# Performance work log

Hardware: AMD Instinct MI355X
Metric: run time of the kernel (lower is better)

The kernel has to match this reference:

```python
import jax, jax.numpy as jnp
import numpy as np

B = 4096          # players (batch)
DEG = 64          # asteroids per player
A = B * DEG       # total asteroids
E = A             # one edge per asteroid (asteroid -> its player)
PD, AD, ED = 5, 3, 7
HID = 64
HEADS = 4
OUT = HID         # GATv2Conv out_channels (concat=False -> mean over heads)
L = 2             # num_layers
NEG_SLOPE = 0.2
LN_EPS = 1e-5


def setup_inputs() -> dict:
    key = jax.random.key(0)
    ks = jax.random.split(key, 20)
    f = jnp.float32
    inp = {}
    inp["player_feat"] = jax.random.normal(ks[0], (B, PD), f)
    inp["asteroid_feat"] = jax.random.normal(ks[1], (A, AD), f)
    src = jnp.arange(E, dtype=jnp.int32)
    dst = src // DEG                      # player batch index per edge
    inp["edge_index"] = jnp.stack([src, dst])  # [2, E] int32
    inp["edge_attr"] = jax.random.normal(ks[2], (E, ED), f)
    sc = 0.1
    # input projections
    inp["Wp"] = jax.random.normal(ks[3], (PD, HID), f) * sc
    inp["bp"] = jnp.zeros((HID,), f)
    inp["Wa"] = jax.random.normal(ks[4], (AD, HID), f) * sc
    inp["ba"] = jnp.zeros((HID,), f)
    # per-layer GATv2 params (stacked over L)
    inp["Wl"] = jax.random.normal(ks[5], (L, HID, HEADS * OUT), f) * sc
    inp["bl"] = jnp.zeros((L, HEADS * OUT), f)
    inp["Wr"] = jax.random.normal(ks[6], (L, HID, HEADS * OUT), f) * sc
    inp["br"] = jnp.zeros((L, HEADS * OUT), f)
    inp["We"] = jax.random.normal(ks[7], (L, ED, HEADS * OUT), f) * sc
    inp["att"] = jax.random.normal(ks[8], (L, HEADS, OUT), f) * sc
    inp["bias"] = jnp.zeros((L, OUT), f)
    inp["ln_g"] = jnp.ones((L, HID), f)
    inp["ln_b"] = jnp.zeros((L, HID), f)
    return inp


def _layer_norm(x, g, b):
    mu = jnp.mean(x, axis=-1, keepdims=True)
    var = jnp.mean(jnp.square(x - mu), axis=-1, keepdims=True)
    return (x - mu) * jax.lax.rsqrt(var + LN_EPS) * g + b


def _gatv2(x, src, dst, edge_attr, Wl, bl, Wr, br, We, att, bias, n_nodes):
    # x: [N, HID]; src/dst: [E]; PyG GATv2Conv, add_self_loops=False, concat=False
    xl = (x @ Wl + bl).reshape(-1, HEADS, OUT)   # source transform
    xr = (x @ Wr + br).reshape(-1, HEADS, OUT)   # target transform
    ea = (edge_attr @ We).reshape(-1, HEADS, OUT)
    e = xl[src] + xr[dst] + ea                   # [E, H, O]
    e = jnp.where(e >= 0, e, NEG_SLOPE * e)      # LeakyReLU(0.2)
    logits = jnp.einsum('eho,ho->eh', e, att)    # [E, H]
    # segment softmax over incoming edges of each target node
    m = jax.ops.segment_max(logits, dst, num_segments=n_nodes)
    al = jnp.exp(logits - m[dst])
    den = jax.ops.segment_sum(al, dst, num_segments=n_nodes)
    alpha = al / den[dst]                        # [E, H]
    msg = alpha[:, :, None] * xl[src]            # [E, H, O]
    out = jax.ops.segment_sum(msg, dst, num_segments=n_nodes)  # [N, H, O]
    return jnp.mean(out, axis=1) + bias          # concat=False -> head mean


def reference(player_feat, asteroid_feat, edge_index, edge_attr,
              Wp, bp, Wa, ba, Wl, bl, Wr, br, We, att, bias, ln_g, ln_b):
    batch = player_feat.shape[0]
    h_p = jax.nn.relu(player_feat @ Wp + bp)
    h_a = jax.nn.relu(asteroid_feat @ Wa + ba)
    x = jnp.concatenate([h_p, h_a], axis=0)      # [N, HID]
    n_nodes = x.shape[0]
    src = edge_index[0] + batch                  # asteroid local -> global idx
    dst = edge_index[1]
    for i in range(L):
        x_new = _gatv2(x, src, dst, edge_attr, Wl[i], bl[i], Wr[i], br[i],
                       We[i], att[i], bias[i], n_nodes)
        x = _layer_norm(x + jax.nn.relu(x_new), ln_g[i], ln_b[i])
    return x[:batch]
```

## Files before the change

kernel.cpp:

```cpp
#include <hip/hip_runtime.h>


typedef __bf16 bf16x8 __attribute__((ext_vector_type(8)));
typedef float  f32x4  __attribute__((ext_vector_type(4)));

union FragU { unsigned short u[8]; bf16x8 v; };

__device__ __forceinline__ float bf2f(unsigned short u) {
    union { unsigned int i; float f; } v; v.i = ((unsigned int)u) << 16; return v.f;
}
__device__ __forceinline__ unsigned short f2bf(float f) {
    union { __bf16 b; unsigned short u; } x; x.b = (__bf16)f; return x.u;
}

#define NEG_SLOPE 0.2f
#define LN_EPS 1e-5f
#define XS 72

struct Smem {
    __align__(16) unsigned short xa[4][64 * XS];
    __align__(16) unsigned short xpb[4][64];
    __align__(16) float alf[4][256];
    float outp[4][256];
    float xp[4][64];
    float afs[4][192];
    float rbs[64], gs[64], bs[64];
};

#define WS_NEED (163840 + 3 * 8192)

__global__ __launch_bounds__(256) void prep_weights(
    const float* __restrict__ Wl, const float* __restrict__ Wr,
    const float* __restrict__ We, const float* __restrict__ bl,
    const float* __restrict__ att, const float* __restrict__ br,
    unsigned short* __restrict__ wlf, unsigned short* __restrict__ wrf,
    unsigned short* __restrict__ wef, f32x4* __restrict__ blq,
    f32x4* __restrict__ attq, f32x4* __restrict__ brq)
{
    int g = blockIdx.x * 256 + threadIdx.x;
    {
        int layer = (g >> 11) & 1, frag = (g >> 8) & 7, t = g & 255;
        int nt = frag >> 1, ko = frag & 1;
        int c = (t >> 6) * 64 + nt * 16 + (t & 15);
        int kb = ko * 32 + ((t >> 4) & 3) * 8;
        const float* srcL = Wl + layer * 16384 + kb * 256 + c;
        const float* srcR = Wr + layer * 16384 + kb * 256 + c;
        FragU fl, fr;
        #pragma unroll
        for (int jj = 0; jj < 8; ++jj) {
            fl.u[jj] = f2bf(srcL[jj * 256]);
            fr.u[jj] = f2bf(srcR[jj * 256]);
        }
        *reinterpret_cast<bf16x8*>(&wlf[g * 8]) = fl.v;
        *reinterpret_cast<bf16x8*>(&wrf[g * 8]) = fr.v;
    }
    if (g < 2048) {
        int l2 = (g >> 10) & 1, n2 = (g >> 8) & 3, t2 = g & 255;
        int q2 = (t2 >> 4) & 3;
        int c2 = (t2 >> 6) * 64 + n2 * 16 + (t2 & 15);
        FragU fe;
        #pragma unroll
        for (int j2 = 0; j2 < 8; ++j2)
            fe.u[j2] = (q2 == 0 && j2 < 7) ? f2bf(We[l2 * 1792 + j2 * 256 + c2])
                                           : (unsigned short)0;
        *reinterpret_cast<bf16x8*>(&wef[g * 8]) = fe.v;
    }
    if (g < 512) {
        int lyr = g >> 8, tt = g & 255;
        int hb = (tt >> 6) * 64, mm = tt & 15;
        f32x4 b, a, r;
        #pragma unroll
        for (int n = 0; n < 4; ++n) {
            int cc = hb + n * 16 + mm;
            b[n] = bl[lyr * 256 + cc];
            a[n] = att[lyr * 256 + cc];
            r[n] = br[lyr * 256 + cc];
        }
        blq[g] = b; attq[g] = a; brq[g] = r;
    }
}

template <bool WS>
__global__ __launch_bounds__(256) void gnn_main(
    const float* __restrict__ pf, const float* __restrict__ af,
    const float* __restrict__ eat, const float* __restrict__ Wp,
    const float* __restrict__ bp, const float* __restrict__ Wa,
    const float* __restrict__ ba, const float* __restrict__ Wl,
    const float* __restrict__ bl, const float* __restrict__ Wr,
    const float* __restrict__ br, const float* __restrict__ We,
    const float* __restrict__ att, const float* __restrict__ bias,
    const float* __restrict__ lng, const float* __restrict__ lnb,
    const unsigned short* __restrict__ wlf, const unsigned short* __restrict__ wrf,
    const unsigned short* __restrict__ wef, const f32x4* __restrict__ blq,
    const f32x4* __restrict__ attq, const f32x4* __restrict__ brq,
    float* __restrict__ out)
{
    __shared__ Smem sm;
    const int p0 = blockIdx.x * 4, t = threadIdx.x;
    const int w = t >> 6, l = t & 63, q = l >> 4, m = l & 15;
    const int cbase = w * 64;

    #pragma unroll
    for (int it = 0; it < 3; ++it) {
        int idx = it * 256 + t;
        int pl = idx / 192, o = idx - pl * 192;
        sm.afs[pl][o] = af[(p0 + pl) * 192 + o];
    }
    if (t < 64) {
        sm.rbs[t] = fmaxf(bias[t], 0.f);
        sm.gs[t] = lng[t];
        sm.bs[t] = lnb[t];
    }
    {
        int pl = w, tt = l;
        float acc = bp[tt];
        #pragma unroll
        for (int d = 0; d < 5; ++d) acc += pf[(p0 + pl) * 5 + d] * Wp[d * 64 + tt];
        float xp0 = fmaxf(acc, 0.f);
        sm.xp[pl][tt] = xp0;
        sm.xpb[pl][tt] = f2bf(xp0);
    }
    __syncthreads();
    {
        const int pl = w, k = l;
        float wa0 = Wa[k], wa1 = Wa[64 + k], wa2 = Wa[128 + k], bak = ba[k];
        #pragma unroll
        for (int j = 0; j < 64; ++j) {
            float acc = bak + sm.afs[pl][j * 3] * wa0 + sm.afs[pl][j * 3 + 1] * wa1
                      + sm.afs[pl][j * 3 + 2] * wa2;
            sm.xa[pl][j * XS + k] = f2bf(fmaxf(acc, 0.f));
        }
    }
    #pragma unroll
    for (int it = 0; it < 8; ++it) {
        int idx = it * 256 + t;
        int pl = idx >> 9, jd = idx & 511, j = jd >> 3, d = jd & 7;
        sm.xa[pl][j * XS + 64 + d] = (d < 7) ? f2bf(eat[((p0 + pl) * 64 + j) * 7 + d])
                                             : (unsigned short)0;
    }
    __syncthreads();

    for (int layer = 0; layer < 2; ++layer) {
        f32x4 blv, atv, brv;
        if constexpr (WS) {
            blv = blq[layer * 256 + t];
            atv = attq[layer * 256 + t];
            brv = brq[layer * 256 + t];
        } else {
            #pragma unroll
            for (int nt = 0; nt < 4; ++nt) {
                int c = cbase + nt * 16 + m;
                blv[nt] = bl[layer * 256 + c];
                atv[nt] = att[layer * 256 + c];
                brv[nt] = br[layer * 256 + c];
            }
        }

        float bx[4][4];
        {
            FragU xf0[4], xf1[4];
            #pragma unroll
            for (int pl = 0; pl < 4; ++pl) {
                xf0[pl].v = *reinterpret_cast<const bf16x8*>(&sm.xpb[pl][q * 8]);
                xf1[pl].v = *reinterpret_cast<const bf16x8*>(&sm.xpb[pl][32 + q * 8]);
            }
            #pragma unroll
            for (int nt = 0; nt < 4; ++nt) {
                FragU r0, r1;
                if constexpr (WS) {
                    r0.v = *reinterpret_cast<const bf16x8*>(&wrf[((layer * 8 + nt * 2 + 0) * 256 + t) * 8]);
                    r1.v = *reinterpret_cast<const bf16x8*>(&wrf[((layer * 8 + nt * 2 + 1) * 256 + t) * 8]);
                } else {
                    int c = cbase + nt * 16 + m;
                    #pragma unroll
                    for (int jj = 0; jj < 8; ++jj) {
                        r0.u[jj] = f2bf(Wr[layer * 16384 + (q * 8 + jj) * 256 + c]);
                        r1.u[jj] = f2bf(Wr[layer * 16384 + (32 + q * 8 + jj) * 256 + c]);
                    }
                }
                #pragma unroll
                for (int pl = 0; pl < 4; ++pl) {
                    f32x4 cx = { brv[nt], brv[nt], brv[nt], brv[nt] };
                    cx = __builtin_amdgcn_mfma_f32_16x16x32_bf16(xf0[pl].v, r0.v, cx, 0, 0, 0);
                    cx = __builtin_amdgcn_mfma_f32_16x16x32_bf16(xf1[pl].v, r1.v, cx, 0, 0, 0);
                    bx[pl][nt] = blv[nt] + cx[0];
                }
            }
        }

        FragU bfr[8];
        bf16x8 ebf[4];
        if constexpr (WS) {
            #pragma unroll
            for (int f = 0; f < 8; ++f)
                bfr[f].v = *reinterpret_cast<const bf16x8*>(&wlf[((layer * 8 + f) * 256 + t) * 8]);
            #pragma unroll
            for (int nt = 0; nt < 4; ++nt)
                ebf[nt] = *reinterpret_cast<const bf16x8*>(&wef[((layer * 4 + nt) * 256 + t) * 8]);
        } else {
            const float* Wli = Wl + layer * 16384;
            #pragma unroll
            for (int nt = 0; nt < 4; ++nt) {
                int c = cbase + nt * 16 + m;
                #pragma unroll
                for (int ko = 0; ko < 2; ++ko) {
                    int kb = ko * 32 + q * 8;
                    #pragma unroll
                    for (int jj = 0; jj < 8; ++jj)
                        bfr[nt * 2 + ko].u[jj] = f2bf(Wli[(kb + jj) * 256 + c]);
                }
                FragU e;
                #pragma unroll
                for (int jj = 0; jj < 8; ++jj)
                    e.u[jj] = (q == 0 && jj < 7) ? f2bf(We[layer * 1792 + jj * 256 + c])
                                                 : (unsigned short)0;
                ebf[nt] = e.v;
            }
        }

        const bool b0 = (m & 1) != 0, b1 = (m & 2) != 0;
        const bool b2 = (m & 4) != 0, b3 = (m & 8) != 0;
        float P[4][4];
        #pragma unroll
        for (int mt = 0; mt < 4; ++mt) {
            const int row = mt * 16 + m;
            #pragma unroll
            for (int pl = 0; pl < 4; ++pl) {
                bf16x8 a0 = *reinterpret_cast<const bf16x8*>(&sm.xa[pl][row * XS + q * 8]);
                bf16x8 a1 = *reinterpret_cast<const bf16x8*>(&sm.xa[pl][row * XS + 32 + q * 8]);
                bf16x8 a2 = *reinterpret_cast<const bf16x8*>(&sm.xa[pl][row * XS + 64]);
                float lp4[4] = { 0.f, 0.f, 0.f, 0.f };
                #pragma unroll
                for (int nt = 0; nt < 4; ++nt) {
                    f32x4 acc = { bx[pl][nt], bx[pl][nt], bx[pl][nt], bx[pl][nt] };
                    acc = __builtin_amdgcn_mfma_f32_16x16x32_bf16(a0, bfr[nt * 2 + 0].v, acc, 0, 0, 0);
                    acc = __builtin_amdgcn_mfma_f32_16x16x32_bf16(a1, bfr[nt * 2 + 1].v, acc, 0, 0, 0);
                    f32x4 ef = __builtin_amdgcn_mfma_f32_16x16x32_bf16(a2, ebf[nt], acc, 0, 0, 0);
                    #pragma unroll
                    for (int r = 0; r < 4; ++r) {
                        float ev = ef[r];
                        ev = fmaxf(ev, NEG_SLOPE * ev);
                        lp4[r] += ev * atv[nt];
                    }
                }
                float e0k = b0 ? lp4[1] : lp4[0], e0s = b0 ? lp4[0] : lp4[1];
                float ea = e0k + __shfl_xor(e0s, 1, 64);
                float e1k = b0 ? lp4[3] : lp4[2], e1s = b0 ? lp4[2] : lp4[3];
                float eb = e1k + __shfl_xor(e1s, 1, 64);
                float fk = b1 ? eb : ea, fs = b1 ? ea : eb;
                P[pl][mt] = fk + __shfl_xor(fs, 2, 64);
            }
        }

        float rden[4];
        #pragma unroll
        for (int pl = 0; pl < 4; ++pl) {
            float g0k = b2 ? P[pl][1] : P[pl][0], g0s = b2 ? P[pl][0] : P[pl][1];
            float ga = g0k + __shfl_xor(g0s, 4, 64);
            float g1k = b2 ? P[pl][3] : P[pl][2], g1s = b2 ? P[pl][2] : P[pl][3];
            float gb = g1k + __shfl_xor(g1s, 4, 64);
            float hk = b3 ? gb : ga, hs = b3 ? ga : gb;
            float lg = hk + __shfl_xor(hs, 8, 64);
            float al = __expf(lg);
            float den = al;
            #pragma unroll
            for (int msk = 1; msk <= 32; msk <<= 1) den += __shfl_xor(den, msk, 64);
            rden[pl] = 1.f / den;
            const int rj = ((m >> 2) * 16) + (q * 4) + (m & 3);
            sm.alf[pl][w * 64 + rj] = al;
        }
        __builtin_amdgcn_wave_barrier();

        #pragma unroll
        for (int pl = 0; pl < 4; ++pl) {
            const f32x4* alv = reinterpret_cast<const f32x4*>(&sm.alf[pl][cbase]);
            f32x4 al4[4];
            #pragma unroll
            for (int mt = 0; mt < 4; ++mt) al4[mt] = alv[mt * 4 + q];
            float s[4] = { 0.f, 0.f, 0.f, 0.f };
            #pragma unroll
            for (int mt = 0; mt < 4; ++mt) {
                const int row = mt * 16 + m;
                bf16x8 a0 = *reinterpret_cast<const bf16x8*>(&sm.xa[pl][row * XS + q * 8]);
                bf16x8 a1 = *reinterpret_cast<const bf16x8*>(&sm.xa[pl][row * XS + 32 + q * 8]);
                #pragma unroll
                for (int nt = 0; nt < 4; ++nt) {
                    f32x4 c1 = { bx[pl][nt], bx[pl][nt], bx[pl][nt], bx[pl][nt] };
                    c1 = __builtin_amdgcn_mfma_f32_16x16x32_bf16(a0, bfr[nt * 2 + 0].v, c1, 0, 0, 0);
                    c1 = __builtin_amdgcn_mfma_f32_16x16x32_bf16(a1, bfr[nt * 2 + 1].v, c1, 0, 0, 0);
                    s[nt] += al4[mt][0] * c1[0] + al4[mt][1] * c1[1]
                           + al4[mt][2] * c1[2] + al4[mt][3] * c1[3];
                }
            }
            #pragma unroll
            for (int nt = 0; nt < 4; ++nt) {
                float sv = s[nt];
                sv += __shfl_xor(sv, 16, 64);
                sv += __shfl_xor(sv, 32, 64);
                if (q == 0)
                    sm.outp[pl][cbase + nt * 16 + m] = sv * rden[pl] - (bx[pl][nt] - blv[nt]);
            }
        }
        __syncthreads();

        if (layer == 0) {
            #pragma unroll
            for (int half = 0; half < 2; ++half) {
                const int g = t >> 1, pl = half * 2 + (g >> 6), j = g & 63, part = t & 1;
                unsigned short* rowp = &sm.xa[pl][j * XS + part * 32];
                FragU A0, A1, A2, A3;
                A0.v = *reinterpret_cast<const bf16x8*>(rowp);
                A1.v = *reinterpret_cast<const bf16x8*>(rowp + 8);
                A2.v = *reinterpret_cast<const bf16x8*>(rowp + 16);
                A3.v = *reinterpret_cast<const bf16x8*>(rowp + 24);
                float v[32], sum = 0.f, sq = 0.f;
                #pragma unroll
                for (int i = 0; i < 32; ++i) {
                    unsigned short us = (i < 8) ? A0.u[i] : (i < 16) ? A1.u[i - 8]
                                      : (i < 24) ? A2.u[i - 16] : A3.u[i - 24];
                    float x = bf2f(us) + sm.rbs[part * 32 + i];
                    v[i] = x; sum += x; sq += x * x;
                }
                sum += __shfl_xor(sum, 1, 64); sq += __shfl_xor(sq, 1, 64);
                float mu = sum * (1.f / 64.f);
                float var = sq * (1.f / 64.f) - mu * mu;
                float rs = rsqrtf(var + LN_EPS);
                FragU O0, O1, O2, O3;
                #pragma unroll
                for (int i = 0; i < 32; ++i) {
                    int col = part * 32 + i;
                    unsigned short ub = f2bf((v[i] - mu) * rs * sm.gs[col] + sm.bs[col]);
                    if (i < 8) O0.u[i] = ub;
                    else if (i < 16) O1.u[i - 8] = ub;
                    else if (i < 24) O2.u[i - 16] = ub;
                    else O3.u[i - 24] = ub;
                }
                *reinterpret_cast<bf16x8*>(rowp) = O0.v;
                *reinterpret_cast<bf16x8*>(rowp + 8) = O1.v;
                *reinterpret_cast<bf16x8*>(rowp + 16) = O2.v;
                *reinterpret_cast<bf16x8*>(rowp + 24) = O3.v;
            }
            {
                const int pl = w, tt = l;
                float xnew = 0.25f * (sm.outp[pl][tt] + sm.outp[pl][64 + tt]
                                    + sm.outp[pl][128 + tt] + sm.outp[pl][192 + tt])
                           + bias[tt];
                float v = sm.xp[pl][tt] + fmaxf(xnew, 0.f);
                float sum = v, sq = v * v;
                #pragma unroll
                for (int msk = 1; msk <= 32; msk <<= 1) {
                    sum += __shfl_xor(sum, msk, 64);
                    sq  += __shfl_xor(sq,  msk, 64);
                }
                float mu = sum * (1.f / 64.f);
                float var = sq * (1.f / 64.f) - mu * mu;
                float y = (v - mu) * rsqrtf(var + LN_EPS) * lng[tt] + lnb[tt];
                sm.xp[pl][tt] = y;
                sm.xpb[pl][tt] = f2bf(y);
            }
            __syncthreads();
        } else {
            {
                const int pl = w, tt = l;
                float xnew = 0.25f * (sm.outp[pl][tt] + sm.outp[pl][64 + tt]
                                    + sm.outp[pl][128 + tt] + sm.outp[pl][192 + tt])
                           + bias[64 + tt];
                float v = sm.xp[pl][tt] + fmaxf(xnew, 0.f);
                float sum = v, sq = v * v;
                #pragma unroll
                for (int msk = 1; msk <= 32; msk <<= 1) {
                    sum += __shfl_xor(sum, msk, 64);
                    sq  += __shfl_xor(sq,  msk, 64);
                }
                float mu = sum * (1.f / 64.f);
                float var = sq * (1.f / 64.f) - mu * mu;
                float y = (v - mu) * rsqrtf(var + LN_EPS) * lng[64 + tt] + lnb[64 + tt];
                out[(p0 + pl) * 64 + tt] = y;
            }
        }
    }
}

extern "C" void kernel_launch(void* const* d_in, const int* in_sizes, int n_in,
                              void* d_out, int out_size, void* d_ws, size_t ws_size,
                              hipStream_t stream) {
    const float* pf   = (const float*)d_in[0];
    const float* af   = (const float*)d_in[1];
    const float* eat  = (const float*)d_in[3];
    const float* Wp   = (const float*)d_in[4];
    const float* bp   = (const float*)d_in[5];
    const float* Wa   = (const float*)d_in[6];
    const float* ba   = (const float*)d_in[7];
    const float* Wl   = (const float*)d_in[8];
    const float* bl   = (const float*)d_in[9];
    const float* Wr   = (const float*)d_in[10];
    const float* br   = (const float*)d_in[11];
    const float* We   = (const float*)d_in[12];
    const float* att  = (const float*)d_in[13];
    const float* bias = (const float*)d_in[14];
    const float* lng  = (const float*)d_in[15];
    const float* lnb  = (const float*)d_in[16];
    float* out = (float*)d_out;

    const int B = in_sizes[0] / 5;
    unsigned short* wlf = (unsigned short*)d_ws;
    unsigned short* wrf = wlf + 32768;
    unsigned short* wef = wrf + 32768;
    f32x4* blq  = (f32x4*)((char*)d_ws + 163840);
    f32x4* attq = blq + 512;
    f32x4* brq  = attq + 512;

    if (ws_size >= WS_NEED) {
        prep_weights<<<dim3(16), dim3(256), 0, stream>>>(
            Wl, Wr, We, bl, att, br, wlf, wrf, wef, blq, attq, brq);
        gnn_main<true><<<dim3(B / 4), dim3(256), 0, stream>>>(
            pf, af, eat, Wp, bp, Wa, ba, Wl, bl, Wr, br, We, att, bias, lng, lnb,
            wlf, wrf, wef, blq, attq, brq, out);
    } else {
        gnn_main<false><<<dim3(B / 4), dim3(256), 0, stream>>>(
            pf, af, eat, Wp, bp, Wa, ba, Wl, bl, Wr, br, We, att, bias, lng, lnb,
            wlf, wrf, wef, blq, attq, brq, out);
    }
}
```

Before: 164.6 us.

## Assign one player per wave, looping over heads to drop block-level syncs

Result: slower. 179.1 us (+8.8%).

```diff
diff --git a/kernel.cpp b/kernel.cpp
--- a/kernel.cpp
+++ b/kernel.cpp
@@ -20,8 +20,7 @@
 struct Smem {
     __align__(16) unsigned short xa[4][64 * XS];
     __align__(16) unsigned short xpb[4][64];
-    __align__(16) float alf[4][256];
-    float outp[4][256];
+    __align__(16) float alf[4][64];
     float xp[4][64];
     float afs[4][192];
     float rbs[64], gs[64], bs[64];
@@ -98,141 +97,134 @@
     __shared__ Smem sm;
     const int p0 = blockIdx.x * 4, t = threadIdx.x;
     const int w = t >> 6, l = t & 63, q = l >> 4, m = l & 15;
-    const int cbase = w * 64;
-
-    #pragma unroll
-    for (int it = 0; it < 3; ++it) {
-        int idx = it * 256 + t;
-        int pl = idx / 192, o = idx - pl * 192;
-        sm.afs[pl][o] = af[(p0 + pl) * 192 + o];
-    }
+    const int p = p0 + w;
+
     if (t < 64) {
         sm.rbs[t] = fmaxf(bias[t], 0.f);
         sm.gs[t] = lng[t];
         sm.bs[t] = lnb[t];
     }
+    #pragma unroll
+    for (int it = 0; it < 3; ++it)
+        sm.afs[w][it * 64 + l] = af[p * 192 + it * 64 + l];
     {
-        int pl = w, tt = l;
-        float acc = bp[tt];
+        float acc = bp[l];
         #pragma unroll
-        for (int d = 0; d < 5; ++d) acc += pf[(p0 + pl) * 5 + d] * Wp[d * 64 + tt];
+        for (int d = 0; d < 5; ++d) acc += pf[p * 5 + d] * Wp[d * 64 + l];
         float xp0 = fmaxf(acc, 0.f);
-        sm.xp[pl][tt] = xp0;
-        sm.xpb[pl][tt] = f2bf(xp0);
-    }
-    __syncthreads();
+        sm.xp[w][l] = xp0;
+        sm.xpb[w][l] = f2bf(xp0);
+    }
+    __builtin_amdgcn_wave_barrier();
     {
-        const int pl = w, k = l;
+        const int k = l;
         float wa0 = Wa[k], wa1 = Wa[64 + k], wa2 = Wa[128 + k], bak = ba[k];
         #pragma unroll
         for (int j = 0; j < 64; ++j) {
-            float acc = bak + sm.afs[pl][j * 3] * wa0 + sm.afs[pl][j * 3 + 1] * wa1
-                      + sm.afs[pl][j * 3 + 2] * wa2;
-            sm.xa[pl][j * XS + k] = f2bf(fmaxf(acc, 0.f));
+            float acc = bak + sm.afs[w][j * 3] * wa0 + sm.afs[w][j * 3 + 1] * wa1
+                      + sm.afs[w][j * 3 + 2] * wa2;
+            sm.xa[w][j * XS + k] = f2bf(fmaxf(acc, 0.f));
         }
     }
     #pragma unroll
     for (int it = 0; it < 8; ++it) {
-        int idx = it * 256 + t;
-        int pl = idx >> 9, jd = idx & 511, j = jd >> 3, d = jd & 7;
-        sm.xa[pl][j * XS + 64 + d] = (d < 7) ? f2bf(eat[((p0 + pl) * 64 + j) * 7 + d])
-                                             : (unsigned short)0;
+        int idx = it * 64 + l, j = idx >> 3, d = idx & 7;
+        sm.xa[w][j * XS + 64 + d] = (d < 7) ? f2bf(eat[(p * 64 + j) * 7 + d])
+                                            : (unsigned short)0;
     }
     __syncthreads();
 
+    const bool b0 = (m & 1) != 0, b1 = (m & 2) != 0;
+    const bool b2 = (m & 4) != 0, b3 = (m & 8) != 0;
+
     for (int layer = 0; layer < 2; ++layer) {
-        f32x4 blv, atv, brv;
-        if constexpr (WS) {
-            blv = blq[layer * 256 + t];
-            atv = attq[layer * 256 + t];
-            brv = brq[layer * 256 + t];
-        } else {
-            #pragma unroll
-            for (int nt = 0; nt < 4; ++nt) {
-                int c = cbase + nt * 16 + m;
-                blv[nt] = bl[layer * 256 + c];
-                atv[nt] = att[layer * 256 + c];
-                brv[nt] = br[layer * 256 + c];
-            }
-        }
-
-        float bx[4][4];
-        {
-            FragU xf0[4], xf1[4];
-            #pragma unroll
-            for (int pl = 0; pl < 4; ++pl) {
-                xf0[pl].v = *reinterpret_cast<const bf16x8*>(&sm.xpb[pl][q * 8]);
-                xf1[pl].v = *reinterpret_cast<const bf16x8*>(&sm.xpb[pl][32 + q * 8]);
-            }
-            #pragma unroll
-            for (int nt = 0; nt < 4; ++nt) {
-                FragU r0, r1;
-                if constexpr (WS) {
-                    r0.v = *reinterpret_cast<const bf16x8*>(&wrf[((layer * 8 + nt * 2 + 0) * 256 + t) * 8]);
-                    r1.v = *reinterpret_cast<const bf16x8*>(&wrf[((layer * 8 + nt * 2 + 1) * 256 + t) * 8]);
-                } else {
-                    int c = cbase + nt * 16 + m;
+        float macc[4] = { 0.f, 0.f, 0.f, 0.f };
+
+        for (int h = 0; h < 4; ++h) {
+            const int ti = h * 64 + l;
+
+            f32x4 blv, atv, brv;
+            if constexpr (WS) {
+                blv = blq[layer * 256 + ti];
+                atv = attq[layer * 256 + ti];
+                brv = brq[layer * 256 + ti];
+            } else {
+                #pragma unroll
+                for (int nt = 0; nt < 4; ++nt) {
+                    int c = h * 64 + nt * 16 + m;
+                    blv[nt] = bl[layer * 256 + c];
+                    atv[nt] = att[layer * 256 + c];
+                    brv[nt] = br[layer * 256 + c];
+                }
+            }
+
+            float bxv[4];
+            {
+                FragU xf0, xf1;
+                xf0.v = *reinterpret_cast<const bf16x8*>(&sm.xpb[w][q * 8]);
+                xf1.v = *reinterpret_cast<const bf16x8*>(&sm.xpb[w][32 + q * 8]);
+                #pragma unroll
+                for (int nt = 0; nt < 4; ++nt) {
+                    FragU r0, r1;
+                    if constexpr (WS) {
+                        r0.v = *reinterpret_cast<const bf16x8*>(&wrf[((layer * 8 + nt * 2 + 0) * 256 + ti) * 8]);
+                        r1.v = *reinterpret_cast<const bf16x8*>(&wrf[((layer * 8 + nt * 2 + 1) * 256 + ti) * 8]);
+                    } else {
+                        int c = h * 64 + nt * 16 + m;
+                        #pragma unroll
+                        for (int jj = 0; jj < 8; ++jj) {
+                            r0.u[jj] = f2bf(Wr[layer * 16384 + (q * 8 + jj) * 256 + c]);
+                            r1.u[jj] = f2bf(Wr[layer * 16384 + (32 + q * 8 + jj) * 256 + c]);
+                        }
+                    }
+                    f32x4 cx = { brv[nt], brv[nt], brv[nt], brv[nt] };
+                    cx = __builtin_amdgcn_mfma_f32_16x16x32_bf16(xf0.v, r0.v, cx, 0, 0, 0);
+                    cx = __builtin_amdgcn_mfma_f32_16x16x32_bf16(xf1.v, r1.v, cx, 0, 0, 0);
+                    bxv[nt] = blv[nt] + cx[0];
+                }
+            }
+
+            FragU bfr[8];
+            bf16x8 ebf[4];
+            if constexpr (WS) {
+                #pragma unroll
+                for (int f = 0; f < 8; ++f)
+                    bfr[f].v = *reinterpret_cast<const bf16x8*>(&wlf[((layer * 8 + f) * 256 + ti) * 8]);
+                #pragma unroll
+                for (int nt = 0; nt < 4; ++nt)
+                    ebf[nt] = *reinterpret_cast<const bf16x8*>(&wef[((layer * 4 + nt) * 256 + ti) * 8]);
+            } else {
+                const float* Wli = Wl + layer * 16384;
+                #pragma unroll
+                for (int nt = 0; nt < 4; ++nt) {
+                    int c = h * 64 + nt * 16 + m;
                     #pragma unroll
-                    for (int jj = 0; jj < 8; ++jj) {
-                        r0.u[jj] = f2bf(Wr[layer * 16384 + (q * 8 + jj) * 256 + c]);
-                        r1.u[jj] = f2bf(Wr[layer * 16384 + (32 + q * 8 + jj) * 256 + c]);
+                    for (int ko = 0; ko < 2; ++ko) {
+                        int kb = ko * 32 + q * 8;
+                        #pragma unroll
+                        for (int jj = 0; jj < 8; ++jj)
+                            bfr[nt * 2 + ko].u[jj] = f2bf(Wli[(kb + jj) * 256 + c]);
                     }
-                }
-                #pragma unroll
-                for (int pl = 0; pl < 4; ++pl) {
-                    f32x4 cx = { brv[nt], brv[nt], brv[nt], brv[nt] };
-                    cx = __builtin_amdgcn_mfma_f32_16x16x32_bf16(xf0[pl].v, r0.v, cx, 0, 0, 0);
-                    cx = __builtin_amdgcn_mfma_f32_16x16x32_bf16(xf1[pl].v, r1.v, cx, 0, 0, 0);
-                    bx[pl][nt] = blv[nt] + cx[0];
-                }
-            }
-        }
-
-        FragU bfr[8];
-        bf16x8 ebf[4];
-        if constexpr (WS) {
-            #pragma unroll
-            for (int f = 0; f < 8; ++f)
-                bfr[f].v = *reinterpret_cast<const bf16x8*>(&wlf[((layer * 8 + f) * 256 + t) * 8]);
-            #pragma unroll
-            for (int nt = 0; nt < 4; ++nt)
-                ebf[nt] = *reinterpret_cast<const bf16x8*>(&wef[((layer * 4 + nt) * 256 + t) * 8]);
-        } else {
-            const float* Wli = Wl + layer * 16384;
-            #pragma unroll
-            for (int nt = 0; nt < 4; ++nt) {
-                int c = cbase + nt * 16 + m;
-                #pragma unroll
-                for (int ko = 0; ko < 2; ++ko) {
-                    int kb = ko * 32 + q * 8;
+                    FragU e;
                     #pragma unroll
                     for (int jj = 0; jj < 8; ++jj)
-                        bfr[nt * 2 + ko].u[jj] = f2bf(Wli[(kb + jj) * 256 + c]);
-                }
-                FragU e;
-                #pragma unroll
-                for (int jj = 0; jj < 8; ++jj)
-                    e.u[jj] = (q == 0 && jj < 7) ? f2bf(We[layer * 1792 + jj * 256 + c])
-                                                 : (unsigned short)0;
-                ebf[nt] = e.v;
-            }
-        }
-
-        const bool b0 = (m & 1) != 0, b1 = (m & 2) != 0;
-        const bool b2 = (m & 4) != 0, b3 = (m & 8) != 0;
-        float P[4][4];
-        #pragma unroll
-        for (int mt = 0; mt < 4; ++mt) {
-            const int row = mt * 16 + m;
+                        e.u[jj] = (q == 0 && jj < 7) ? f2bf(We[layer * 1792 + jj * 256 + c])
+                                                     : (unsigned short)0;
+                    ebf[nt] = e.v;
+                }
+            }
+
+            float P[4];
             #pragma unroll
-            for (int pl = 0; pl < 4; ++pl) {
-                bf16x8 a0 = *reinterpret_cast<const bf16x8*>(&sm.xa[pl][row * XS + q * 8]);
-                bf16x8 a1 = *reinterpret_cast<const bf16x8*>(&sm.xa[pl][row * XS + 32 + q * 8]);
-                bf16x8 a2 = *reinterpret_cast<const bf16x8*>(&sm.xa[pl][row * XS + 64]);
+            for (int mt = 0; mt < 4; ++mt) {
+                const int row = mt * 16 + m;
+                bf16x8 a0 = *reinterpret_cast<const bf16x8*>(&sm.xa[w][row * XS + q * 8]);
+                bf16x8 a1 = *reinterpret_cast<const bf16x8*>(&sm.xa[w][row * XS + 32 + q * 8]);
+                bf16x8 a2 = *reinterpret_cast<const bf16x8*>(&sm.xa[w][row * XS + 64]);
                 float lp4[4] = { 0.f, 0.f, 0.f, 0.f };
                 #pragma unroll
                 for (int nt = 0; nt < 4; ++nt) {
-                    f32x4 acc = { bx[pl][nt], bx[pl][nt], bx[pl][nt], bx[pl][nt] };
+                    f32x4 acc = { bxv[nt], bxv[nt], bxv[nt], bxv[nt] };
                     acc = __builtin_amdgcn_mfma_f32_16x16x32_bf16(a0, bfr[nt * 2 + 0].v, acc, 0, 0, 0);
                     acc = __builtin_amdgcn_mfma_f32_16x16x32_bf16(a1, bfr[nt * 2 + 1].v, acc, 0, 0, 0);
                     f32x4 ef = __builtin_amdgcn_mfma_f32_16x16x32_bf16(a2, ebf[nt], acc, 0, 0, 0);
@@ -248,66 +240,92 @@
                 float e1k = b0 ? lp4[3] : lp4[2], e1s = b0 ? lp4[2] : lp4[3];
                 float eb = e1k + __shfl_xor(e1s, 1, 64);
                 float fk = b1 ? eb : ea, fs = b1 ? ea : eb;
-                P[pl][mt] = fk + __shfl_xor(fs, 2, 64);
-            }
-        }
-
-        float rden[4];
-        #pragma unroll
-        for (int pl = 0; pl < 4; ++pl) {
-            float g0k = b2 ? P[pl][1] : P[pl][0], g0s = b2 ? P[pl][0] : P[pl][1];
-            float ga = g0k + __shfl_xor(g0s, 4, 64);
-            float g1k = b2 ? P[pl][3] : P[pl][2], g1s = b2 ? P[pl][2] : P[pl][3];
-            float gb = g1k + __shfl_xor(g1s, 4, 64);
-            float hk = b3 ? gb : ga, hs = b3 ? ga : gb;
-            float lg = hk + __shfl_xor(hs, 8, 64);
-            float al = __expf(lg);
-            float den = al;
-            #pragma unroll
-            for (int msk = 1; msk <= 32; msk <<= 1) den += __shfl_xor(den, msk, 64);
-            rden[pl] = 1.f / den;
-            const int rj = ((m >> 2) * 16) + (q * 4) + (m & 3);
-            sm.alf[pl][w * 64 + rj] = al;
-        }
-        __builtin_amdgcn_wave_barrier();
-
-        #pragma unroll
-        for (int pl = 0; pl < 4; ++pl) {
-            const f32x4* alv = reinterpret_cast<const f32x4*>(&sm.alf[pl][cbase]);
-            f32x4 al4[4];
-            #pragma unroll
-            for (int mt = 0; mt < 4; ++mt) al4[mt] = alv[mt * 4 + q];
-            float s[4] = { 0.f, 0.f, 0.f, 0.f };
-            #pragma unroll
-            for (int mt = 0; mt < 4; ++mt) {
-                const int row = mt * 16 + m;
-                bf16x8 a0 = *reinterpret_cast<const bf16x8*>(&sm.xa[pl][row * XS + q * 8]);
-                bf16x8 a1 = *reinterpret_cast<const bf16x8*>(&sm.xa[pl][row * XS + 32 + q * 8]);
+                P[mt] = fk + __shfl_xor(fs, 2, 64);
+            }
+
+            float rden;
+            {
+                float g0k = b2 ? P[1] : P[0], g0s = b2 ? P[0] : P[1];
+                float ga = g0k + __shfl_xor(g0s, 4, 64);
+                float g1k = b2 ? P[3] : P[2], g1s = b2 ? P[2] : P[3];
+                float gb = g1k + __shfl_xor(g1s, 4, 64);
+                float hk = b3 ? gb : ga, hs = b3 ? ga : gb;
+                float lg = hk + __shfl_xor(hs, 8, 64);
+                float al = __expf(lg);
+                float den = al;
+                #pragma unroll
+                for (int msk = 1; msk <= 32; msk <<= 1) den += __shfl_xor(den, msk, 64);
+                rden = 1.f / den;
+                const int rj = ((m >> 2) * 16) + (q * 4) + (m & 3);
+                sm.alf[w][rj] = al;
+            }
+            __builtin_amdgcn_wave_barrier();
+
+            {
+                const f32x4* alv = reinterpret_cast<const f32x4*>(&sm.alf[w][0]);
+                f32x4 al4[4];
+                #pragma unroll
+                for (int mt = 0; mt < 4; ++mt) al4[mt] = alv[mt * 4 + q];
+                float s[4] = { 0.f, 0.f, 0.f, 0.f };
+                #pragma unroll
+                for (int mt = 0; mt < 4; ++mt) {
+                    const int row = mt * 16 + m;
+                    bf16x8 a0 = *reinterpret_cast<const bf16x8*>(&sm.xa[w][row * XS + q * 8]);
+                    bf16x8 a1 = *reinterpret_cast<const bf16x8*>(&sm.xa[w][row * XS + 32 + q * 8]);
+                    #pragma unroll
+                    for (int nt = 0; nt < 4; ++nt) {
+                        f32x4 c1 = { bxv[nt], bxv[nt], bxv[nt], bxv[nt] };
+                        c1 = __builtin_amdgcn_mfma_f32_16x16x32_bf16(a0, bfr[nt * 2 + 0].v, c1, 0, 0, 0);
+                        c1 = __builtin_amdgcn_mfma_f32_16x16x32_bf16(a1, bfr[nt * 2 + 1].v, c1, 0, 0, 0);
+                        s[nt] += al4[mt][0] * c1[0] + al4[mt][1] * c1[1]
+                               + al4[mt][2] * c1[2] + al4[mt][3] * c1[3];
+                    }
+                }
                 #pragma unroll
                 for (int nt = 0; nt < 4; ++nt) {
-                    f32x4 c1 = { bx[pl][nt], bx[pl][nt], bx[pl][nt], bx[pl][nt] };
-                    c1 = __builtin_amdgcn_mfma_f32_16x16x32_bf16(a0, bfr[nt * 2 + 0].v, c1, 0, 0, 0);
-                    c1 = __builtin_amdgcn_mfma_f32_16x16x32_bf16(a1, bfr[nt * 2 + 1].v, c1, 0, 0, 0);
-                    s[nt] += al4[mt][0] * c1[0] + al4[mt][1] * c1[1]
-                           + al4[mt][2] * c1[2] + al4[mt][3] * c1[3];
-                }
-            }
+                    float sv = s[nt];
+                    sv += __shfl_xor(sv, 16, 64);
+                    sv += __shfl_xor(sv, 32, 64);
+                    macc[nt] += sv * rden - (bxv[nt] - blv[nt]);
+                }
+            }
+            __builtin_amdgcn_wave_barrier();
+        }
+
+        {
+            float v4[4], sum = 0.f, sq = 0.f;
             #pragma unroll
             for (int nt = 0; nt < 4; ++nt) {
-                float sv = s[nt];
-                sv += __shfl_xor(sv, 16, 64);
-                sv += __shfl_xor(sv, 32, 64);
-                if (q == 0)
-                    sm.outp[pl][cbase + nt * 16 + m] = sv * rden[pl] - (bx[pl][nt] - blv[nt]);
-            }
-        }
-        __syncthreads();
+                int col = nt * 16 + m;
+                float xnew = 0.25f * macc[nt] + bias[layer * 64 + col];
+                float v = sm.xp[w][col] + fmaxf(xnew, 0.f);
+                v4[nt] = v; sum += v; sq += v * v;
+            }
+            #pragma unroll
+            for (int msk = 1; msk <= 8; msk <<= 1) {
+                sum += __shfl_xor(sum, msk, 64);
+                sq  += __shfl_xor(sq,  msk, 64);
+            }
+            float mu = sum * (1.f / 64.f);
+            float var = sq * (1.f / 64.f) - mu * mu;
+            float rs = rsqrtf(var + LN_EPS);
+            #pragma unroll
+            for (int nt = 0; nt < 4; ++nt) {
+                int col = nt * 16 + m;
+                float y = (v4[nt] - mu) * rs * lng[layer * 64 + col] + lnb[layer * 64 + col];
+                if (layer == 0) {
+                    if (q == 0) { sm.xp[w][col] = y; sm.xpb[w][col] = f2bf(y); }
+                } else {
+                    if (q == 0) out[p * 64 + col] = y;
+                }
+            }
+        }
 
         if (layer == 0) {
             #pragma unroll
-            for (int half = 0; half < 2; ++half) {
-                const int g = t >> 1, pl = half * 2 + (g >> 6), j = g & 63, part = t & 1;
-                unsigned short* rowp = &sm.xa[pl][j * XS + part * 32];
+            for (int hp = 0; hp < 2; ++hp) {
+                const int j = hp * 32 + (l >> 1), part = l & 1;
+                unsigned short* rowp = &sm.xa[w][j * XS + part * 32];
                 FragU A0, A1, A2, A3;
                 A0.v = *reinterpret_cast<const bf16x8*>(rowp);
                 A1.v = *reinterpret_cast<const bf16x8*>(rowp + 8);
@@ -340,43 +358,7 @@
                 *reinterpret_cast<bf16x8*>(rowp + 16) = O2.v;
                 *reinterpret_cast<bf16x8*>(rowp + 24) = O3.v;
             }
-            {
-                const int pl = w, tt = l;
-                float xnew = 0.25f * (sm.outp[pl][tt] + sm.outp[pl][64 + tt]
-                                    + sm.outp[pl][128 + tt] + sm.outp[pl][192 + tt])
-                           + bias[tt];
-                float v = sm.xp[pl][tt] + fmaxf(xnew, 0.f);
-                float sum = v, sq = v * v;
-                #pragma unroll
-                for (int msk = 1; msk <= 32; msk <<= 1) {
-                    sum += __shfl_xor(sum, msk, 64);
-                    sq  += __shfl_xor(sq,  msk, 64);
-                }
-                float mu = sum * (1.f / 64.f);
-                float var = sq * (1.f / 64.f) - mu * mu;
-                float y = (v - mu) * rsqrtf(var + LN_EPS) * lng[tt] + lnb[tt];
-                sm.xp[pl][tt] = y;
-                sm.xpb[pl][tt] = f2bf(y);
-            }
-            __syncthreads();
-        } else {
-            {
-                const int pl = w, tt = l;
-                float xnew = 0.25f * (sm.outp[pl][tt] + sm.outp[pl][64 + tt]
-                                    + sm.outp[pl][128 + tt] + sm.outp[pl][192 + tt])
-                           + bias[64 + tt];
-                float v = sm.xp[pl][tt] + fmaxf(xnew, 0.f);
-                float sum = v, sq = v * v;
-                #pragma unroll
-                for (int msk = 1; msk <= 32; msk <<= 1) {
-                    sum += __shfl_xor(sum, msk, 64);
-                    sq  += __shfl_xor(sq,  msk, 64);
-                }
-                float mu = sum * (1.f / 64.f);
-                float var = sq * (1.f / 64.f) - mu * mu;
-                float y = (v - mu) * rsqrtf(var + LN_EPS) * lng[64 + tt] + lnb[64 + tt];
-                out[(p0 + pl) * 64 + tt] = y;
-            }
+            __builtin_amdgcn_wave_barrier();
         }
     }
 }
```

## Shrink LDS footprint with bf16 aliased alpha/output buffer and register-held player state

Applied to the files above, without the earlier changes.

Result: no change. 165.1 us (+0.3%).

```diff
diff --git a/kernel.cpp b/kernel.cpp
--- a/kernel.cpp
+++ b/kernel.cpp
@@ -3,6 +3,7 @@
 
 typedef __bf16 bf16x8 __attribute__((ext_vector_type(8)));
 typedef float  f32x4  __attribute__((ext_vector_type(4)));
+typedef unsigned short u16x4 __attribute__((ext_vector_type(4)));
 
 union FragU { unsigned short u[8]; bf16x8 v; };
 
@@ -20,10 +21,7 @@
 struct Smem {
     __align__(16) unsigned short xa[4][64 * XS];
     __align__(16) unsigned short xpb[4][64];
-    __align__(16) float alf[4][256];
-    float outp[4][256];
-    float xp[4][64];
-    float afs[4][192];
+    __align__(16) unsigned short alfoutp[4][256];
     float rbs[64], gs[64], bs[64];
 };
 
@@ -99,36 +97,30 @@
     const int p0 = blockIdx.x * 4, t = threadIdx.x;
     const int w = t >> 6, l = t & 63, q = l >> 4, m = l & 15;
     const int cbase = w * 64;
-
-    #pragma unroll
-    for (int it = 0; it < 3; ++it) {
-        int idx = it * 256 + t;
-        int pl = idx / 192, o = idx - pl * 192;
-        sm.afs[pl][o] = af[(p0 + pl) * 192 + o];
-    }
+    const int p = p0 + w;
+
     if (t < 64) {
         sm.rbs[t] = fmaxf(bias[t], 0.f);
         sm.gs[t] = lng[t];
         sm.bs[t] = lnb[t];
     }
+    float xpreg;
     {
-        int pl = w, tt = l;
-        float acc = bp[tt];
-        #pragma unroll
-        for (int d = 0; d < 5; ++d) acc += pf[(p0 + pl) * 5 + d] * Wp[d * 64 + tt];
-        float xp0 = fmaxf(acc, 0.f);
-        sm.xp[pl][tt] = xp0;
-        sm.xpb[pl][tt] = f2bf(xp0);
-    }
-    __syncthreads();
+        float acc = bp[l];
+        #pragma unroll
+        for (int d = 0; d < 5; ++d) acc += pf[p * 5 + d] * Wp[d * 64 + l];
+        xpreg = fmaxf(acc, 0.f);
+        sm.xpb[w][l] = f2bf(xpreg);
+    }
     {
-        const int pl = w, k = l;
+        const float* afp = af + p * 192;
+        const int k = l;
         float wa0 = Wa[k], wa1 = Wa[64 + k], wa2 = Wa[128 + k], bak = ba[k];
         #pragma unroll
         for (int j = 0; j < 64; ++j) {
-            float acc = bak + sm.afs[pl][j * 3] * wa0 + sm.afs[pl][j * 3 + 1] * wa1
-                      + sm.afs[pl][j * 3 + 2] * wa2;
-            sm.xa[pl][j * XS + k] = f2bf(fmaxf(acc, 0.f));
+            float acc = bak + afp[j * 3] * wa0 + afp[j * 3 + 1] * wa1
+                      + afp[j * 3 + 2] * wa2;
+            sm.xa[w][j * XS + k] = f2bf(fmaxf(acc, 0.f));
         }
     }
     #pragma unroll
@@ -267,16 +259,19 @@
             for (int msk = 1; msk <= 32; msk <<= 1) den += __shfl_xor(den, msk, 64);
             rden[pl] = 1.f / den;
             const int rj = ((m >> 2) * 16) + (q * 4) + (m & 3);
-            sm.alf[pl][w * 64 + rj] = al;
+            sm.alfoutp[pl][w * 64 + rj] = f2bf(al);
         }
         __builtin_amdgcn_wave_barrier();
 
         #pragma unroll
         for (int pl = 0; pl < 4; ++pl) {
-            const f32x4* alv = reinterpret_cast<const f32x4*>(&sm.alf[pl][cbase]);
+            const u16x4* alv = reinterpret_cast<const u16x4*>(&sm.alfoutp[pl][cbase]);
             f32x4 al4[4];
             #pragma unroll
-            for (int mt = 0; mt < 4; ++mt) al4[mt] = alv[mt * 4 + q];
+            for (int mt = 0; mt < 4; ++mt) {
+                u16x4 a4 = alv[mt * 4 + q];
+                al4[mt] = (f32x4){ bf2f(a4[0]), bf2f(a4[1]), bf2f(a4[2]), bf2f(a4[3]) };
+            }
             float s[4] = { 0.f, 0.f, 0.f, 0.f };
             #pragma unroll
             for (int mt = 0; mt < 4; ++mt) {
@@ -298,7 +293,8 @@
                 sv += __shfl_xor(sv, 16, 64);
                 sv += __shfl_xor(sv, 32, 64);
                 if (q == 0)
-                    sm.outp[pl][cbase + nt * 16 + m] = sv * rden[pl] - (bx[pl][nt] - blv[nt]);
+                    sm.alfoutp[pl][cbase + nt * 16 + m]
+                        = f2bf(sv * rden[pl] - (bx[pl][nt] - blv[nt]));
             }
         }
         __syncthreads();
@@ -341,11 +337,10 @@
                 *reinterpret_cast<bf16x8*>(rowp + 24) = O3.v;
             }
             {
-                const int pl = w, tt = l;
-                float xnew = 0.25f * (sm.outp[pl][tt] + sm.outp[pl][64 + tt]
-                                    + sm.outp[pl][128 + tt] + sm.outp[pl][192 + tt])
-                           + bias[tt];
-                float v = sm.xp[pl][tt] + fmaxf(xnew, 0.f);
+                float xnew = 0.25f * (bf2f(sm.alfoutp[w][l]) + bf2f(sm.alfoutp[w][64 + l])
+                                    + bf2f(sm.alfoutp[w][128 + l]) + bf2f(sm.alfoutp[w][192 + l]))
+                           + bias[l];
+                float v = xpreg + fmaxf(xnew, 0.f);
                 float sum = v, sq = v * v;
                 #pragma unroll
                 for (int msk = 1; msk <= 32; msk <<= 1) {
@@ -354,18 +349,17 @@
                 }
                 float mu = sum * (1.f / 64.f);
                 float var = sq * (1.f / 64.f) - mu * mu;
-                float y = (v - mu) * rsqrtf(var + LN_EPS) * lng[tt] + lnb[tt];
-                sm.xp[pl][tt] = y;
-                sm.xpb[pl][tt] = f2bf(y);
+                float y = (v - mu) * rsqrtf(var + LN_EPS) * lng[l] + lnb[l];
+                xpreg = y;
+                sm.xpb[w][l] = f2bf(y);
             }
             __syncthreads();
         } else {
             {
-                const int pl = w, tt = l;
-                float xnew = 0.25f * (sm.outp[pl][tt] + sm.outp[pl][64 + tt]
-                                    + sm.outp[pl][128 + tt] + sm.outp[pl][192 + tt])
-                           + bias[64 + tt];
-                float v = sm.xp[pl][tt] + fmaxf(xnew, 0.f);
+                float xnew = 0.25f * (bf2f(sm.alfoutp[w][l]) + bf2f(sm.alfoutp[w][64 + l])
+                                    + bf2f(sm.alfoutp[w][128 + l]) + bf2f(sm.alfoutp[w][192 + l]))
+                           + bias[64 + l];
+                float v = xpreg + fmaxf(xnew, 0.f);
                 float sum = v, sq = v * v;
                 #pragma unroll
                 for (int msk = 1; msk <= 32; msk <<= 1) {
@@ -374,8 +368,8 @@
                 }
                 float mu = sum * (1.f / 64.f);
                 float var = sq * (1.f / 64.f) - mu * mu;
-                float y = (v - mu) * rsqrtf(var + LN_EPS) * lng[64 + tt] + lnb[64 + tt];
-                out[(p0 + pl) * 64 + tt] = y;
+                float y = (v - mu) * rsqrtf(var + LN_EPS) * lng[64 + l] + lnb[64 + l];
+                out[p * 64 + l] = y;
             }
         }
     }
```
